# Performance work log

Measured on AMD Instinct MI355X. Metric: run time of the kernel, lower is better.

## Reference

```python
import jax, jax.numpy as jnp
import numpy as np

N = 4096          # nproteins
IN_F = 512        # in_features
OUT_F = 64        # out_features
ALPHA = 0.2       # leakyrelu slope
EPS = 1e-5        # batchnorm eps
NEG = -9e15       # mask fill value from the original code


def setup_inputs() -> dict:
    key = jax.random.key(0)
    k = jax.random.split(key, 5)
    h = jax.random.normal(k[0], (N, IN_F), dtype=jnp.float32)
    # sparse 0/1 adjacency (avg degree ~20) stored dense, as the module expects
    adj = (jax.random.uniform(k[1], (N, N)) < 0.005).astype(jnp.float32)
    half = IN_F // 2
    # xavier_uniform with gain=1.414 ~ U(-b, b), b = gain*sqrt(6/(fan_in+fan_out))
    b_w = 1.414 * np.sqrt(6.0 / (half + OUT_F))
    W1 = jax.random.uniform(k[2], (half, OUT_F), minval=-b_w, maxval=b_w, dtype=jnp.float32)
    W2 = jax.random.uniform(k[3], (half, OUT_F), minval=-b_w, maxval=b_w, dtype=jnp.float32)
    b_a = 1.414 * np.sqrt(6.0 / (2 * OUT_F + 1))
    a = jax.random.uniform(k[4], (2 * OUT_F, 1), minval=-b_a, maxval=b_a, dtype=jnp.float32)
    gamma = jnp.ones((2 * OUT_F,), dtype=jnp.float32)   # bn2 weight
    beta = jnp.zeros((2 * OUT_F,), dtype=jnp.float32)   # bn2 bias
    return {"h": h, "adj": adj, "W1": W1, "W2": W2, "a": a, "gamma": gamma, "beta": beta}


def _lrelu(x):
    return jnp.where(x > 0, x, ALPHA * x)


def reference(h, adj, W1, W2, a, gamma, beta):
    d = h.shape[1] // 2
    Wh1 = h[:, :d] @ W1          # [N, F]
    Wh2 = h[:, d:] @ W2          # [N, F]

    def prep(Wh):
        s1 = Wh @ a[:OUT_F]      # [N, 1]
        s2 = Wh @ a[OUT_F:]      # [N, 1]
        return _lrelu(s1 + s2.T)  # [N, N]

    e1 = prep(Wh1)
    e2 = prep(Wh2)

    adj2 = adj @ adj                               # 2-hop counts [N, N]
    adj2 = adj2 - jnp.diag(jnp.diag(adj2))         # zero the diagonal

    att1 = jax.nn.softmax(jnp.where(adj > 0, e1, NEG), axis=1)
    h_prime1 = att1 @ Wh1                          # [N, F]
    att2 = jax.nn.softmax(jnp.where(adj2 > 0, e2, NEG), axis=1)
    h_prime2 = att2 @ Wh2                          # [N, F]

    hp = jnp.concatenate([h_prime1, h_prime2], axis=-1)  # [N, 2F]
    # BatchNorm1d (training-mode batch stats, biased variance)
    mean = hp.mean(axis=0)
    var = hp.var(axis=0)
    out = gamma * (hp - mean) / jnp.sqrt(var + EPS) + beta
    return _lrelu(out)  # concat=True branch
```

## Files before the change

kernel.cpp:

```cpp
#include <hip/hip_runtime.h>
#include <hip/hip_bf16.h>

#define NN 4096
#define IN_F 512
#define HALF 256
#define FF 64
#define ALPHA 0.2f
#define EPSV 1e-5f
#define CAP1 256
#define CAP2 1024

typedef unsigned long long u64;
typedef unsigned int u32;

__device__ __forceinline__ float lrelu(float x){ return x > 0.f ? x : ALPHA * x; }

__device__ __forceinline__ float wave_fmax(float v){
    #pragma unroll
    for (int off = 32; off; off >>= 1) v = fmaxf(v, __shfl_xor(v, off, 64));
    return v;
}
__device__ __forceinline__ float wave_fsum(float v){
    #pragma unroll
    for (int off = 32; off; off >>= 1) v += __shfl_xor(v, off, 64);
    return v;
}

__device__ __forceinline__ int build_idx(u64 bits, int lane, int cap, int* __restrict__ nbr){
    int pc = __popcll(bits);
    int scan = pc;
    #pragma unroll
    for (int off = 1; off < 64; off <<= 1) {
        int v = __shfl_up(scan, off, 64);
        if (lane >= off) scan += v;
    }
    int total = __shfl(scan, 63, 64);
    int pos = scan - pc;
    while (bits) {
        int b = __builtin_ctzll(bits);
        bits &= bits - 1;
        if (pos < cap) nbr[pos] = (lane << 6) | b;
        ++pos;
    }
    return total;
}

__global__ __launch_bounds__(256) void pack_kernel(const float* __restrict__ adj,
                                                   u64* __restrict__ packA) {
    int i = blockIdx.x;
    int tid = threadIdx.x;
    int wave = tid >> 6, lane = tid & 63;
    const float* row = adj + (size_t)i * NN;
    #pragma unroll
    for (int t = 0; t < NN / 256; ++t) {
        int col = t * 256 + tid;
        u64 m = __ballot(row[col] > 0.f);
        if (lane == 0) packA[(size_t)i * 64 + t * 4 + wave] = m;
    }
}

__global__ __launch_bounds__(128) void wh_kernel(const float* __restrict__ h,
                                                 const float* __restrict__ W1,
                                                 const float* __restrict__ W2,
                                                 const float* __restrict__ a,
                                                 float* __restrict__ Wh1,
                                                 float* __restrict__ Wh2,
                                                 float* __restrict__ s11,
                                                 float* __restrict__ s12,
                                                 float* __restrict__ s21,
                                                 float* __restrict__ s22) {
    __shared__ float hs[4 * IN_F];
    int r0 = blockIdx.x * 4;
    int tid = threadIdx.x;
    const float4* hsrc = (const float4*)(h + (size_t)r0 * IN_F);
    float4* hdst = (float4*)hs;
    #pragma unroll
    for (int t = 0; t < 4; ++t) hdst[tid + 128 * t] = hsrc[tid + 128 * t];
    __syncthreads();

    int wave = tid >> 6, f = tid & 63;
    const float* W = wave ? W2 : W1;
    const float* hw = hs + wave * HALF;
    float acc0 = 0.f, acc1 = 0.f, acc2 = 0.f, acc3 = 0.f;
    #pragma unroll 4
    for (int k = 0; k < HALF; ++k) {
        float w = W[k * FF + f];
        acc0 += hw[k] * w;
        acc1 += hw[IN_F + k] * w;
        acc2 += hw[2 * IN_F + k] * w;
        acc3 += hw[3 * IN_F + k] * w;
    }
    float* Wh = wave ? Wh2 : Wh1;
    Wh[(size_t)(r0 + 0) * FF + f] = acc0;
    Wh[(size_t)(r0 + 1) * FF + f] = acc1;
    Wh[(size_t)(r0 + 2) * FF + f] = acc2;
    Wh[(size_t)(r0 + 3) * FF + f] = acc3;

    float a1 = a[f], a2 = a[64 + f];
    #pragma unroll
    for (int r = 0; r < 4; ++r) {
        float acc = (r == 0) ? acc0 : (r == 1) ? acc1 : (r == 2) ? acc2 : acc3;
        float v1 = acc * a1, v2 = acc * a2;
        #pragma unroll
        for (int off = 32; off; off >>= 1) {
            v1 += __shfl_down(v1, off, 64);
            v2 += __shfl_down(v2, off, 64);
        }
        if (f == 0) {
            if (wave == 0) { s11[r0 + r] = v1; s12[r0 + r] = v2; }
            else           { s21[r0 + r] = v1; s22[r0 + r] = v2; }
        }
    }
}

__global__ __launch_bounds__(256) void attn_kernel(const u64* __restrict__ packA,
                                                   const float* __restrict__ Wh1,
                                                   const float* __restrict__ Wh2,
                                                   const float* __restrict__ s11,
                                                   const float* __restrict__ s12,
                                                   const float* __restrict__ s21,
                                                   const float* __restrict__ s22,
                                                   float* __restrict__ hp) {
    __shared__ int   nbr1[CAP1];
    __shared__ float ev1[CAP1];
    __shared__ int   nbr2[CAP2];
    __shared__ float ev2[CAP2];
    __shared__ u64   maskw[3 * 64];
    __shared__ float red[8];
    __shared__ float partial[1024];
    __shared__ int   scnt1, scnt2;

    int i = blockIdx.x;
    int tid = threadIdx.x;
    int w = tid >> 6, lane = tid & 63;

    if (w == 0) {
        int t1 = build_idx(packA[(size_t)i * 64 + lane], lane, CAP1, nbr1);
        if (lane == 0) scnt1 = t1;
    }
    __syncthreads();
    int c1 = min(scnt1, CAP1);

    if (c1 > 0) {
        if (w == 0) {
            float s11i = s11[i];
            float lm = -3.4e38f;
            for (int n = lane; n < c1; n += 64) {
                float e = lrelu(s11i + s12[nbr1[n]]);
                ev1[n] = e;
                lm = fmaxf(lm, e);
            }
            float m = wave_fmax(lm);
            float ls = 0.f;
            for (int n = lane; n < c1; n += 64) {
                float p = __expf(ev1[n] - m);
                ev1[n] = p;
                ls += p;
            }
            float Z = wave_fsum(ls);
            float acc = 0.f;
            #pragma unroll 4
            for (int n = 0; n < c1; ++n)
                acc += ev1[n] * Wh1[(size_t)nbr1[n] * FF + lane];
            hp[(size_t)i * 128 + lane] = acc / Z;
        } else {
            u64 m = 0;
            for (int n = w - 1; n < c1; n += 3)
                m |= packA[(size_t)nbr1[n] * 64 + lane];
            maskw[(w - 1) * 64 + lane] = m;
        }
    } else {
        int g = tid >> 4, fq = (tid & 15) << 2;
        float ax = 0.f, ay = 0.f, az = 0.f, aw = 0.f;
        for (int n = g; n < NN; n += 16) {
            const float4 v = *reinterpret_cast<const float4*>(&Wh1[(size_t)n * FF + fq]);
            ax += v.x; ay += v.y; az += v.z; aw += v.w;
        }
        *reinterpret_cast<float4*>(&partial[tid << 2]) = make_float4(ax, ay, az, aw);
        if (w) maskw[(w - 1) * 64 + lane] = 0;
        __syncthreads();
        if (tid < 64) {
            float s = 0.f;
            #pragma unroll
            for (int g2 = 0; g2 < 16; ++g2) s += partial[g2 * 64 + tid];
            hp[(size_t)i * 128 + tid] = s / (float)NN;
        }
    }
    __syncthreads();

    if (w == 0) {
        u64 word = maskw[lane] | maskw[64 + lane] | maskw[128 + lane];
        if (lane == (i >> 6)) word &= ~(1ull << (i & 63));
        int t2 = build_idx(word, lane, CAP2, nbr2);
        if (lane == 0) scnt2 = t2;
    }
    __syncthreads();
    int c2 = min(scnt2, CAP2);

    float Z2;
    if (c2 > 0) {
        float s21i = s21[i];
        float lm = -3.4e38f;
        for (int n = tid; n < c2; n += 256) {
            float e = lrelu(s21i + s22[nbr2[n]]);
            ev2[n] = e;
            lm = fmaxf(lm, e);
        }
        lm = wave_fmax(lm);
        if (lane == 0) red[w] = lm;
        __syncthreads();
        float mx = fmaxf(fmaxf(red[0], red[1]), fmaxf(red[2], red[3]));
        float ls = 0.f;
        for (int n = tid; n < c2; n += 256) {
            float p = __expf(ev2[n] - mx);
            ev2[n] = p;
            ls += p;
        }
        ls = wave_fsum(ls);
        if (lane == 0) red[4 + w] = ls;
        __syncthreads();
        Z2 = red[4] + red[5] + red[6] + red[7];
    } else {
        Z2 = (float)NN;
    }

    int g = tid >> 4, fq = (tid & 15) << 2;
    float ax = 0.f, ay = 0.f, az = 0.f, aw = 0.f;
    if (c2 > 0) {
        #pragma unroll 4
        for (int n = g; n < c2; n += 16) {
            float wg = ev2[n];
            const float4 v = *reinterpret_cast<const float4*>(&Wh2[(size_t)nbr2[n] * FF + fq]);
            ax += wg * v.x; ay += wg * v.y; az += wg * v.z; aw += wg * v.w;
        }
    } else {
        #pragma unroll 4
        for (int n = g; n < NN; n += 16) {
            const float4 v = *reinterpret_cast<const float4*>(&Wh2[(size_t)n * FF + fq]);
            ax += v.x; ay += v.y; az += v.z; aw += v.w;
        }
    }
    __syncthreads();
    *reinterpret_cast<float4*>(&partial[tid << 2]) = make_float4(ax, ay, az, aw);
    __syncthreads();
    if (tid < 64) {
        float s = 0.f;
        #pragma unroll
        for (int g2 = 0; g2 < 16; ++g2) s += partial[g2 * 64 + tid];
        hp[(size_t)i * 128 + 64 + tid] = s / Z2;
    }
}

__global__ __launch_bounds__(256) void stats_kernel(const float* __restrict__ hp,
                                                    float* __restrict__ ps,
                                                    float* __restrict__ pq) {
    __shared__ float ls[128], lq[128];
    int tid = threadIdx.x;
    if (tid < 128) { ls[tid] = 0.f; lq[tid] = 0.f; }
    __syncthreads();
    float s0 = 0, s1 = 0, s2 = 0, s3 = 0, q0 = 0, q1 = 0, q2 = 0, q3 = 0;
    const float4* hp4 = (const float4*)hp;
    for (size_t idx = (size_t)blockIdx.x * 256 + tid; idx < (size_t)NN * 32;
         idx += (size_t)gridDim.x * 256) {
        float4 v = hp4[idx];
        s0 += v.x; q0 += v.x * v.x;
        s1 += v.y; q1 += v.y * v.y;
        s2 += v.z; q2 += v.z * v.z;
        s3 += v.w; q3 += v.w * v.w;
    }
    int cb = (tid & 31) << 2;
    atomicAdd(&ls[cb + 0], s0); atomicAdd(&lq[cb + 0], q0);
    atomicAdd(&ls[cb + 1], s1); atomicAdd(&lq[cb + 1], q1);
    atomicAdd(&ls[cb + 2], s2); atomicAdd(&lq[cb + 2], q2);
    atomicAdd(&ls[cb + 3], s3); atomicAdd(&lq[cb + 3], q3);
    __syncthreads();
    if (tid < 128) {
        ps[(size_t)blockIdx.x * 128 + tid] = ls[tid];
        pq[(size_t)blockIdx.x * 128 + tid] = lq[tid];
    }
}

__global__ __launch_bounds__(256) void finalize_kernel(const float* __restrict__ ps,
                                                       const float* __restrict__ pq,
                                                       float* __restrict__ colsum,
                                                       float* __restrict__ colsq) {
    int tid = threadIdx.x;
    const float* src = (tid < 128) ? ps : pq;
    int c = tid & 127;
    float s = 0.f;
    #pragma unroll 8
    for (int b = 0; b < 256; ++b) s += src[(size_t)b * 128 + c];
    if (tid < 128) colsum[c] = s;
    else           colsq[c]  = s;
}

__global__ __launch_bounds__(256) void norm_kernel(float* __restrict__ hp,
                                                   const float* __restrict__ colsum,
                                                   const float* __restrict__ colsq,
                                                   const float* __restrict__ gamma,
                                                   const float* __restrict__ beta) {
    size_t idx = (size_t)blockIdx.x * 256 + threadIdx.x;
    if (idx >= (size_t)NN * 32) return;
    int cb = (int)((idx << 2) & 127);
    float4 v = ((const float4*)hp)[idx];
    float r[4] = {v.x, v.y, v.z, v.w};
    #pragma unroll
    for (int t = 0; t < 4; ++t) {
        int c = cb + t;
        float mean = colsum[c] * (1.f / NN);
        float var = colsq[c] * (1.f / NN) - mean * mean;
        float inv = rsqrtf(var + EPSV);
        r[t] = lrelu((r[t] - mean) * inv * gamma[c] + beta[c]);
    }
    ((float4*)hp)[idx] = make_float4(r[0], r[1], r[2], r[3]);
}

extern "C" void kernel_launch(void* const* d_in, const int* in_sizes, int n_in,
                              void* d_out, int out_size, void* d_ws, size_t ws_size,
                              hipStream_t stream) {
    const float* h     = (const float*)d_in[0];
    const float* adj   = (const float*)d_in[1];
    const float* W1    = (const float*)d_in[2];
    const float* W2    = (const float*)d_in[3];
    const float* a     = (const float*)d_in[4];
    const float* gamma = (const float*)d_in[5];
    const float* beta  = (const float*)d_in[6];
    float* hp = (float*)d_out;

    u64* packA  = (u64*)d_ws;
    float* Wh1  = (float*)(packA + (size_t)NN * 64);
    float* Wh2  = Wh1 + (size_t)NN * FF;
    float* s11  = Wh2 + (size_t)NN * FF;
    float* s12  = s11 + NN;
    float* s21  = s12 + NN;
    float* s22  = s21 + NN;
    float* ps   = s22 + NN;
    float* pq   = ps + 256 * 128;
    float* colsum = pq + 256 * 128;
    float* colsq  = colsum + 128;

    pack_kernel<<<NN, 256, 0, stream>>>(adj, packA);
    wh_kernel<<<NN / 4, 128, 0, stream>>>(h, W1, W2, a, Wh1, Wh2, s11, s12, s21, s22);
    attn_kernel<<<NN, 256, 0, stream>>>(packA, Wh1, Wh2, s11, s12, s21, s22, hp);
    stats_kernel<<<256, 256, 0, stream>>>(hp, ps, pq);
    finalize_kernel<<<1, 256, 0, stream>>>(ps, pq, colsum, colsq);
    norm_kernel<<<(NN * 32 + 255) / 256, 256, 0, stream>>>(hp, colsum, colsq, gamma, beta);
}
```

Baseline: 179.2 us.

## Fuse pack and Wh kernels; vectorize neighbor gathers with float4 and padding

Merges the adjacency bit-packing kernel and the Wh projection kernel into a single launch. Block indices select the role, and the Wh part now covers 8 rows per 256-thread block. The neighbor aggregation loops in the attention kernel now load four neighbor indices and weights at a time and do float4 gathers of Wh rows, with the index lists zero-padded to multiples of 16 or 64. The first-hop path splits the 64 features across 16-lane groups and finishes with cross-lane shuffles. The aim is less launch overhead and more memory-level parallelism in the gathers, at the cost of padding writes and extra shuffle work.

```diff
diff --git a/kernel.cpp b/kernel.cpp
--- a/kernel.cpp
+++ b/kernel.cpp
@@ -9,6 +9,7 @@
 #define EPSV 1e-5f
 #define CAP1 256
 #define CAP2 1024
+#define WHB (NN / 8)
 
 typedef unsigned long long u64;
 typedef unsigned int u32;
@@ -45,70 +46,73 @@
     return total;
 }
 
-__global__ __launch_bounds__(256) void pack_kernel(const float* __restrict__ adj,
-                                                   u64* __restrict__ packA) {
-    int i = blockIdx.x;
+__global__ __launch_bounds__(256) void packwh_kernel(const float* __restrict__ adj,
+                                                     u64* __restrict__ packA,
+                                                     const float* __restrict__ h,
+                                                     const float* __restrict__ W1,
+                                                     const float* __restrict__ W2,
+                                                     const float* __restrict__ a,
+                                                     float* __restrict__ Wh1,
+                                                     float* __restrict__ Wh2,
+                                                     float* __restrict__ s11,
+                                                     float* __restrict__ s12,
+                                                     float* __restrict__ s21,
+                                                     float* __restrict__ s22) {
+    __shared__ float hs[8 * IN_F];
     int tid = threadIdx.x;
-    int wave = tid >> 6, lane = tid & 63;
-    const float* row = adj + (size_t)i * NN;
-    #pragma unroll
-    for (int t = 0; t < NN / 256; ++t) {
-        int col = t * 256 + tid;
-        u64 m = __ballot(row[col] > 0.f);
-        if (lane == 0) packA[(size_t)i * 64 + t * 4 + wave] = m;
-    }
-}
-
-__global__ __launch_bounds__(128) void wh_kernel(const float* __restrict__ h,
-                                                 const float* __restrict__ W1,
-                                                 const float* __restrict__ W2,
-                                                 const float* __restrict__ a,
-                                                 float* __restrict__ Wh1,
-                                                 float* __restrict__ Wh2,
-                                                 float* __restrict__ s11,
-                                                 float* __restrict__ s12,
-                                                 float* __restrict__ s21,
-                                                 float* __restrict__ s22) {
-    __shared__ float hs[4 * IN_F];
-    int r0 = blockIdx.x * 4;
-    int tid = threadIdx.x;
-    const float4* hsrc = (const float4*)(h + (size_t)r0 * IN_F);
-    float4* hdst = (float4*)hs;
-    #pragma unroll
-    for (int t = 0; t < 4; ++t) hdst[tid + 128 * t] = hsrc[tid + 128 * t];
-    __syncthreads();
-
-    int wave = tid >> 6, f = tid & 63;
-    const float* W = wave ? W2 : W1;
-    const float* hw = hs + wave * HALF;
-    float acc0 = 0.f, acc1 = 0.f, acc2 = 0.f, acc3 = 0.f;
-    #pragma unroll 4
-    for (int k = 0; k < HALF; ++k) {
-        float w = W[k * FF + f];
-        acc0 += hw[k] * w;
-        acc1 += hw[IN_F + k] * w;
-        acc2 += hw[2 * IN_F + k] * w;
-        acc3 += hw[3 * IN_F + k] * w;
-    }
-    float* Wh = wave ? Wh2 : Wh1;
-    Wh[(size_t)(r0 + 0) * FF + f] = acc0;
-    Wh[(size_t)(r0 + 1) * FF + f] = acc1;
-    Wh[(size_t)(r0 + 2) * FF + f] = acc2;
-    Wh[(size_t)(r0 + 3) * FF + f] = acc3;
-
-    float a1 = a[f], a2 = a[64 + f];
-    #pragma unroll
-    for (int r = 0; r < 4; ++r) {
-        float acc = (r == 0) ? acc0 : (r == 1) ? acc1 : (r == 2) ? acc2 : acc3;
-        float v1 = acc * a1, v2 = acc * a2;
+    if (blockIdx.x < NN) {
+        int i = blockIdx.x;
+        int wave = tid >> 6, lane = tid & 63;
+        const float* row = adj + (size_t)i * NN;
         #pragma unroll
-        for (int off = 32; off; off >>= 1) {
-            v1 += __shfl_down(v1, off, 64);
-            v2 += __shfl_down(v2, off, 64);
-        }
-        if (f == 0) {
-            if (wave == 0) { s11[r0 + r] = v1; s12[r0 + r] = v2; }
-            else           { s21[r0 + r] = v1; s22[r0 + r] = v2; }
+        for (int t = 0; t < NN / 256; ++t) {
+            int col = t * 256 + tid;
+            u64 m = __ballot(row[col] > 0.f);
+            if (lane == 0) packA[(size_t)i * 64 + t * 4 + wave] = m;
+        }
+    } else {
+        int r0 = (blockIdx.x - NN) * 8;
+        const float4* hsrc = (const float4*)(h + (size_t)r0 * IN_F);
+        float4* hdst = (float4*)hs;
+        #pragma unroll
+        for (int t = 0; t < 4; ++t) hdst[tid + 256 * t] = hsrc[tid + 256 * t];
+        __syncthreads();
+
+        int w = tid >> 6, f = tid & 63;
+        int br2 = w >> 1;
+        int rbase = (w & 1) * 4;
+        const float* W = br2 ? W2 : W1;
+        const float* hw = hs + rbase * IN_F + br2 * HALF;
+        float acc0 = 0.f, acc1 = 0.f, acc2 = 0.f, acc3 = 0.f;
+        #pragma unroll 4
+        for (int k = 0; k < HALF; ++k) {
+            float wt = W[k * FF + f];
+            acc0 += hw[k] * wt;
+            acc1 += hw[IN_F + k] * wt;
+            acc2 += hw[2 * IN_F + k] * wt;
+            acc3 += hw[3 * IN_F + k] * wt;
+        }
+        float* Wh = br2 ? Wh2 : Wh1;
+        int rr = r0 + rbase;
+        Wh[(size_t)(rr + 0) * FF + f] = acc0;
+        Wh[(size_t)(rr + 1) * FF + f] = acc1;
+        Wh[(size_t)(rr + 2) * FF + f] = acc2;
+        Wh[(size_t)(rr + 3) * FF + f] = acc3;
+
+        float a1 = a[f], a2 = a[64 + f];
+        #pragma unroll
+        for (int r = 0; r < 4; ++r) {
+            float acc = (r == 0) ? acc0 : (r == 1) ? acc1 : (r == 2) ? acc2 : acc3;
+            float v1 = acc * a1, v2 = acc * a2;
+            #pragma unroll
+            for (int off = 32; off; off >>= 1) {
+                v1 += __shfl_down(v1, off, 64);
+                v2 += __shfl_down(v2, off, 64);
+            }
+            if (f == 0) {
+                if (br2 == 0) { s11[rr + r] = v1; s12[rr + r] = v2; }
+                else          { s21[rr + r] = v1; s22[rr + r] = v2; }
+            }
         }
     }
 }
@@ -143,6 +147,8 @@
 
     if (c1 > 0) {
         if (w == 0) {
+            int c1p = (c1 + 15) & ~15;
+            for (int n = c1 + lane; n < c1p; n += 64) { nbr1[n] = 0; ev1[n] = 0.f; }
             float s11i = s11[i];
             float lm = -3.4e38f;
             for (int n = lane; n < c1; n += 64) {
@@ -157,33 +163,49 @@
                 ev1[n] = p;
                 ls += p;
             }
-            float Z = wave_fsum(ls);
-            float acc = 0.f;
-            #pragma unroll 4
-            for (int n = 0; n < c1; ++n)
-                acc += ev1[n] * Wh1[(size_t)nbr1[n] * FF + lane];
-            hp[(size_t)i * 128 + lane] = acc / Z;
+            float invZ = 1.f / wave_fsum(ls);
+            int g = lane >> 4, fq = (lane & 15) << 2;
+            float ax = 0.f, ay = 0.f, az = 0.f, aw = 0.f;
+            for (int n = g * 4; n < c1p; n += 16) {
+                int4   nb = *(const int4*)&nbr1[n];
+                float4 wv = *(const float4*)&ev1[n];
+                float4 q0 = *(const float4*)&Wh1[nb.x * FF + fq];
+                float4 q1 = *(const float4*)&Wh1[nb.y * FF + fq];
+                float4 q2 = *(const float4*)&Wh1[nb.z * FF + fq];
+                float4 q3 = *(const float4*)&Wh1[nb.w * FF + fq];
+                ax += wv.x * q0.x + wv.y * q1.x + wv.z * q2.x + wv.w * q3.x;
+                ay += wv.x * q0.y + wv.y * q1.y + wv.z * q2.y + wv.w * q3.y;
+                az += wv.x * q0.z + wv.y * q1.z + wv.z * q2.z + wv.w * q3.z;
+                aw += wv.x * q0.w + wv.y * q1.w + wv.z * q2.w + wv.w * q3.w;
+            }
+            ax += __shfl_xor(ax, 16, 64); ax += __shfl_xor(ax, 32, 64);
+            ay += __shfl_xor(ay, 16, 64); ay += __shfl_xor(ay, 32, 64);
+            az += __shfl_xor(az, 16, 64); az += __shfl_xor(az, 32, 64);
+            aw += __shfl_xor(aw, 16, 64); aw += __shfl_xor(aw, 32, 64);
+            if (g == 0)
+                *(float4*)&hp[(size_t)i * 128 + fq] =
+                    make_float4(ax * invZ, ay * invZ, az * invZ, aw * invZ);
         } else {
             u64 m = 0;
             for (int n = w - 1; n < c1; n += 3)
-                m |= packA[(size_t)nbr1[n] * 64 + lane];
+                m |= packA[nbr1[n] * 64 + lane];
             maskw[(w - 1) * 64 + lane] = m;
         }
     } else {
         int g = tid >> 4, fq = (tid & 15) << 2;
         float ax = 0.f, ay = 0.f, az = 0.f, aw = 0.f;
         for (int n = g; n < NN; n += 16) {
-            const float4 v = *reinterpret_cast<const float4*>(&Wh1[(size_t)n * FF + fq]);
+            float4 v = *(const float4*)&Wh1[n * FF + fq];
             ax += v.x; ay += v.y; az += v.z; aw += v.w;
         }
-        *reinterpret_cast<float4*>(&partial[tid << 2]) = make_float4(ax, ay, az, aw);
+        *(float4*)&partial[tid << 2] = make_float4(ax, ay, az, aw);
         if (w) maskw[(w - 1) * 64 + lane] = 0;
         __syncthreads();
         if (tid < 64) {
             float s = 0.f;
             #pragma unroll
             for (int g2 = 0; g2 < 16; ++g2) s += partial[g2 * 64 + tid];
-            hp[(size_t)i * 128 + tid] = s / (float)NN;
+            hp[(size_t)i * 128 + tid] = s * (1.f / NN);
         }
     }
     __syncthreads();
@@ -196,8 +218,9 @@
     }
     __syncthreads();
     int c2 = min(scnt2, CAP2);
-
-    float Z2;
+    int c2p = (c2 + 63) & ~63;
+
+    float Z2inv;
     if (c2 > 0) {
         float s21i = s21[i];
         float lm = -3.4e38f;
@@ -216,38 +239,43 @@
             ev2[n] = p;
             ls += p;
         }
+        for (int n = c2 + tid; n < c2p; n += 256) { ev2[n] = 0.f; nbr2[n] = 0; }
         ls = wave_fsum(ls);
         if (lane == 0) red[4 + w] = ls;
         __syncthreads();
-        Z2 = red[4] + red[5] + red[6] + red[7];
+        Z2inv = 1.f / (red[4] + red[5] + red[6] + red[7]);
     } else {
-        Z2 = (float)NN;
+        Z2inv = 1.f / (float)NN;
     }
 
     int g = tid >> 4, fq = (tid & 15) << 2;
     float ax = 0.f, ay = 0.f, az = 0.f, aw = 0.f;
     if (c2 > 0) {
-        #pragma unroll 4
-        for (int n = g; n < c2; n += 16) {
-            float wg = ev2[n];
-            const float4 v = *reinterpret_cast<const float4*>(&Wh2[(size_t)nbr2[n] * FF + fq]);
-            ax += wg * v.x; ay += wg * v.y; az += wg * v.z; aw += wg * v.w;
+        for (int n = g * 4; n < c2p; n += 64) {
+            int4   nb = *(const int4*)&nbr2[n];
+            float4 wv = *(const float4*)&ev2[n];
+            float4 q0 = *(const float4*)&Wh2[nb.x * FF + fq];
+            float4 q1 = *(const float4*)&Wh2[nb.y * FF + fq];
+            float4 q2 = *(const float4*)&Wh2[nb.z * FF + fq];
+            float4 q3 = *(const float4*)&Wh2[nb.w * FF + fq];
+            ax += wv.x * q0.x + wv.y * q1.x + wv.z * q2.x + wv.w * q3.x;
+            ay += wv.x * q0.y + wv.y * q1.y + wv.z * q2.y + wv.w * q3.y;
+            az += wv.x * q0.z + wv.y * q1.z + wv.z * q2.z + wv.w * q3.z;
+            aw += wv.x * q0.w + wv.y * q1.w + wv.z * q2.w + wv.w * q3.w;
         }
     } else {
-        #pragma unroll 4
         for (int n = g; n < NN; n += 16) {
-            const float4 v = *reinterpret_cast<const float4*>(&Wh2[(size_t)n * FF + fq]);
+            float4 v = *(const float4*)&Wh2[n * FF + fq];
             ax += v.x; ay += v.y; az += v.z; aw += v.w;
         }
     }
-    __syncthreads();
-    *reinterpret_cast<float4*>(&partial[tid << 2]) = make_float4(ax, ay, az, aw);
+    *(float4*)&partial[tid << 2] = make_float4(ax, ay, az, aw);
     __syncthreads();
     if (tid < 64) {
         float s = 0.f;
         #pragma unroll
         for (int g2 = 0; g2 < 16; ++g2) s += partial[g2 * 64 + tid];
-        hp[(size_t)i * 128 + 64 + tid] = s / Z2;
+        hp[(size_t)i * 128 + 64 + tid] = s * Z2inv;
     }
 }
 
@@ -339,8 +367,8 @@
     float* colsum = pq + 256 * 128;
     float* colsq  = colsum + 128;
 
-    pack_kernel<<<NN, 256, 0, stream>>>(adj, packA);
-    wh_kernel<<<NN / 4, 128, 0, stream>>>(h, W1, W2, a, Wh1, Wh2, s11, s12, s21, s22);
+    packwh_kernel<<<NN + WHB, 256, 0, stream>>>(adj, packA, h, W1, W2, a,
+                                                Wh1, Wh2, s11, s12, s21, s22);
     attn_kernel<<<NN, 256, 0, stream>>>(packA, Wh1, Wh2, s11, s12, s21, s22, hp);
     stats_kernel<<<256, 256, 0, stream>>>(hp, ps, pq);
     finalize_kernel<<<1, 256, 0, stream>>>(ps, pq, colsum, colsq);
```

New measurement: 183.3 us. 2.3% more time.
